# Performance work log

Measured on AMD Instinct MI355X. Metric: run time of the kernel, lower is better.

## Reference

```python
import jax, jax.numpy as jnp
import numpy as np

KERNEL_SIZE = 3  # matches init kwarg kernel_size=3, blurring_type='median'


def setup_inputs() -> dict:
    key = jax.random.key(0)
    x = jax.random.uniform(key, (64, 224, 224, 3), dtype=jnp.float32)
    return {"x": x}


def reference(x):
    # cv2.medianBlur with ksize=3: 3x3 windowed median per pixel per channel,
    # with replicated borders (cv2 uses BORDER_REPLICATE for medianBlur).
    k = KERNEL_SIZE
    p = k // 2
    B, H, W, C = x.shape
    xp = jnp.pad(x, ((0, 0), (p, p), (p, p), (0, 0)), mode="edge")
    # Stack the k*k shifted views -> [B, H, W, C, k*k]; loop is over the fixed
    # 3x3 stencil (9 taps), not over data dims.
    patches = jnp.stack(
        [xp[:, i:i + H, j:j + W, :] for i in range(k) for j in range(k)],
        axis=-1,
    )
    return jnp.median(patches, axis=-1)
```

## Files before the change

### kernel.cpp

```cpp
#include <hip/hip_runtime.h>


__device__ __forceinline__ float min3f(float a, float b, float c) {
    return fminf(fminf(a, b), c);
}
__device__ __forceinline__ float max3f(float a, float b, float c) {
    return fmaxf(fmaxf(a, b), c);
}
__device__ __forceinline__ float med3f(float a, float b, float c) {
    return __builtin_amdgcn_fmed3f(a, b, c);
}

__global__ __launch_bounds__(256) void median3x3_v4(
    const float* __restrict__ in, float* __restrict__ out)
{
    const int W = 224, H = 224;
    const int ROWF   = W * 3;
    const int CHUNKS = ROWF / 4;
    const int NXCD = 8;
    const int BANDS = 9408 / NXCD;

    int bid  = blockIdx.x;
    int virt = (bid & (NXCD - 1)) * BANDS + (bid >> 3);

    int t   = virt * 256 + threadIdx.x;
    int ci  = t % CHUNKS;
    int rid = t / CHUNKS;
    int h   = rid % H;

    const float* rowC = in + (size_t)rid * ROWF;
    const float* rowU = rowC + ((h > 0)     ? -ROWF : 0);
    const float* rowD = rowC + ((h < H - 1) ?  ROWF : 0);

    const int li  = (ci > 0)          ? ci - 1 : 0;
    const int riq = (ci < CHUNKS - 1) ? ci + 1 : CHUNKS - 1;
    const bool first = (ci == 0), last = (ci == CHUNKS - 1);

    float v[3][10];
    const float* rows[3] = { rowU, rowC, rowD };
    #pragma unroll
    for (int r = 0; r < 3; ++r) {
        float4 L = ((const float4*)rows[r])[li];
        float4 M = ((const float4*)rows[r])[ci];
        float4 R = ((const float4*)rows[r])[riq];
        v[r][0] = first ? M.x : L.y;
        v[r][1] = first ? M.y : L.z;
        v[r][2] = first ? M.z : L.w;
        v[r][3] = M.x;
        v[r][4] = M.y;
        v[r][5] = M.z;
        v[r][6] = M.w;
        v[r][7] = last ? M.y : R.x;
        v[r][8] = last ? M.z : R.y;
        v[r][9] = last ? M.w : R.z;
    }

    float lo[10], me[10], hi[10];
    #pragma unroll
    for (int q = 0; q < 10; ++q) {
        lo[q] = min3f(v[0][q], v[1][q], v[2][q]);
        me[q] = med3f(v[0][q], v[1][q], v[2][q]);
        hi[q] = max3f(v[0][q], v[1][q], v[2][q]);
    }

    float o0, o1, o2, o3;
    {
        float a = max3f(lo[0], lo[3], lo[6]);
        float b = med3f(me[0], me[3], me[6]);
        float c = min3f(hi[0], hi[3], hi[6]);
        o0 = med3f(a, b, c);
    }
    {
        float a = max3f(lo[1], lo[4], lo[7]);
        float b = med3f(me[1], me[4], me[7]);
        float c = min3f(hi[1], hi[4], hi[7]);
        o1 = med3f(a, b, c);
    }
    {
        float a = max3f(lo[2], lo[5], lo[8]);
        float b = med3f(me[2], me[5], me[8]);
        float c = min3f(hi[2], hi[5], hi[8]);
        o2 = med3f(a, b, c);
    }
    {
        float a = max3f(lo[3], lo[6], lo[9]);
        float b = med3f(me[3], me[6], me[9]);
        float c = min3f(hi[3], hi[6], hi[9]);
        o3 = med3f(a, b, c);
    }

    ((float4*)(out + (size_t)rid * ROWF))[ci] = make_float4(o0, o1, o2, o3);
}

extern "C" void kernel_launch(void* const* d_in, const int* in_sizes, int n_in,
                              void* d_out, int out_size, void* d_ws, size_t ws_size,
                              hipStream_t stream) {
    const float* x = (const float*)d_in[0];
    float* out     = (float*)d_out;

    const int grid  = 9408;
    const int block = 256;
    median3x3_v4<<<grid, block, 0, stream>>>(x, out);
}
```

Baseline: 18.84 us.

## Compute four output rows per thread to reuse vertical neighbor loads

Each thread now loads six input rows and produces four consecutive output rows, instead of loading three rows for a single output row. The grid shrinks by a factor of four. This cuts redundant global and L2 loads from overlapping vertical windows from 3x to 1.5x. In exchange, fewer threads run and register pressure per thread rises, which may reduce occupancy and latency hiding on a memory-bound kernel.

```diff
diff --git a/kernel.cpp b/kernel.cpp
--- a/kernel.cpp
+++ b/kernel.cpp
@@ -11,38 +11,41 @@
     return __builtin_amdgcn_fmed3f(a, b, c);
 }
 
-__global__ __launch_bounds__(256) void median3x3_v4(
+__global__ __launch_bounds__(256) void median3x3_r4(
     const float* __restrict__ in, float* __restrict__ out)
 {
     const int W = 224, H = 224;
     const int ROWF   = W * 3;
     const int CHUNKS = ROWF / 4;
-    const int NXCD = 8;
-    const int BANDS = 9408 / NXCD;
+    const int GROUPS = H / 4;
+    const int NXCD   = 8;
+    const int BAND   = 2352 / NXCD;
 
     int bid  = blockIdx.x;
-    int virt = (bid & (NXCD - 1)) * BANDS + (bid >> 3);
+    int virt = (bid & (NXCD - 1)) * BAND + (bid >> 3);
 
-    int t   = virt * 256 + threadIdx.x;
-    int ci  = t % CHUNKS;
-    int rid = t / CHUNKS;
-    int h   = rid % H;
+    int t    = virt * 256 + threadIdx.x;
+    int ci   = t % CHUNKS;
+    int rest = t / CHUNKS;
+    int g    = rest % GROUPS;
+    int b    = rest / GROUPS;
+    int r0   = g * 4;
 
-    const float* rowC = in + (size_t)rid * ROWF;
-    const float* rowU = rowC + ((h > 0)     ? -ROWF : 0);
-    const float* rowD = rowC + ((h < H - 1) ?  ROWF : 0);
+    const float* img = in + (size_t)b * H * ROWF;
 
     const int li  = (ci > 0)          ? ci - 1 : 0;
     const int riq = (ci < CHUNKS - 1) ? ci + 1 : CHUNKS - 1;
     const bool first = (ci == 0), last = (ci == CHUNKS - 1);
 
-    float v[3][10];
-    const float* rows[3] = { rowU, rowC, rowD };
+    float v[6][10];
     #pragma unroll
-    for (int r = 0; r < 3; ++r) {
-        float4 L = ((const float4*)rows[r])[li];
-        float4 M = ((const float4*)rows[r])[ci];
-        float4 R = ((const float4*)rows[r])[riq];
+    for (int r = 0; r < 6; ++r) {
+        int h = r0 + r - 1;
+        h = (h < 0) ? 0 : ((h > H - 1) ? H - 1 : h);
+        const float4* rp = (const float4*)(img + (size_t)h * ROWF);
+        float4 L = rp[li];
+        float4 M = rp[ci];
+        float4 R = rp[riq];
         v[r][0] = first ? M.x : L.y;
         v[r][1] = first ? M.y : L.z;
         v[r][2] = first ? M.z : L.w;
@@ -55,41 +58,32 @@
         v[r][9] = last ? M.w : R.z;
     }
 
-    float lo[10], me[10], hi[10];
+    float* oimg = out + (size_t)b * H * ROWF;
+
     #pragma unroll
-    for (int q = 0; q < 10; ++q) {
-        lo[q] = min3f(v[0][q], v[1][q], v[2][q]);
-        me[q] = med3f(v[0][q], v[1][q], v[2][q]);
-        hi[q] = max3f(v[0][q], v[1][q], v[2][q]);
+    for (int k = 0; k < 4; ++k) {
+        float lo[10], me[10], hi[10];
+        #pragma unroll
+        for (int q = 0; q < 10; ++q) {
+            lo[q] = min3f(v[k][q], v[k + 1][q], v[k + 2][q]);
+            me[q] = med3f(v[k][q], v[k + 1][q], v[k + 2][q]);
+            hi[q] = max3f(v[k][q], v[k + 1][q], v[k + 2][q]);
+        }
+        float4 o;
+        o.x = med3f(max3f(lo[0], lo[3], lo[6]),
+                    med3f(me[0], me[3], me[6]),
+                    min3f(hi[0], hi[3], hi[6]));
+        o.y = med3f(max3f(lo[1], lo[4], lo[7]),
+                    med3f(me[1], me[4], me[7]),
+                    min3f(hi[1], hi[4], hi[7]));
+        o.z = med3f(max3f(lo[2], lo[5], lo[8]),
+                    med3f(me[2], me[5], me[8]),
+                    min3f(hi[2], hi[5], hi[8]));
+        o.w = med3f(max3f(lo[3], lo[6], lo[9]),
+                    med3f(me[3], me[6], me[9]),
+                    min3f(hi[3], hi[6], hi[9]));
+        ((float4*)(oimg + (size_t)(r0 + k) * ROWF))[ci] = o;
     }
-
-    float o0, o1, o2, o3;
-    {
-        float a = max3f(lo[0], lo[3], lo[6]);
-        float b = med3f(me[0], me[3], me[6]);
-        float c = min3f(hi[0], hi[3], hi[6]);
-        o0 = med3f(a, b, c);
-    }
-    {
-        float a = max3f(lo[1], lo[4], lo[7]);
-        float b = med3f(me[1], me[4], me[7]);
-        float c = min3f(hi[1], hi[4], hi[7]);
-        o1 = med3f(a, b, c);
-    }
-    {
-        float a = max3f(lo[2], lo[5], lo[8]);
-        float b = med3f(me[2], me[5], me[8]);
-        float c = min3f(hi[2], hi[5], hi[8]);
-        o2 = med3f(a, b, c);
-    }
-    {
-        float a = max3f(lo[3], lo[6], lo[9]);
-        float b = med3f(me[3], me[6], me[9]);
-        float c = min3f(hi[3], hi[6], hi[9]);
-        o3 = med3f(a, b, c);
-    }
-
-    ((float4*)(out + (size_t)rid * ROWF))[ci] = make_float4(o0, o1, o2, o3);
 }
 
 extern "C" void kernel_launch(void* const* d_in, const int* in_sizes, int n_in,
@@ -98,7 +92,7 @@
     const float* x = (const float*)d_in[0];
     float* out     = (float*)d_out;
 
-    const int grid  = 9408;
+    const int grid  = 2352;
     const int block = 256;
-    median3x3_v4<<<grid, block, 0, stream>>>(x, out);
+    median3x3_r4<<<grid, block, 0, stream>>>(x, out);
 }
```

Result: faster. 18.34 us (-2.6%).
